# Performance work log

Hardware: AMD Instinct MI355X
Metric: run time of the kernel (lower is better)

## Reference

```python
import jax, jax.numpy as jnp
import numpy as np

N_NODES = 100000
N_BATCH = 16384
N_EDGES = 524288
D_FEAT = 256


def setup_inputs() -> dict:
    key = jax.random.key(0)
    k1, k2, k3, k4 = jax.random.split(key, 4)
    features = jax.random.normal(k1, (N_NODES, D_FEAT), dtype=jnp.float32)
    # flat ragged neighbor list: neigh_idx[e] is a node id, segment_ids[e] is
    # the batch-node it belongs to (sorted, i.e. CSR-style ragged layout)
    neigh_idx = jax.random.randint(k2, (N_EDGES,), 0, N_NODES, dtype=jnp.int64)
    segment_ids = jnp.sort(jax.random.randint(k3, (N_EDGES,), 0, N_BATCH, dtype=jnp.int64))
    self_feats = jax.random.normal(k4, (N_BATCH, D_FEAT), dtype=jnp.float32)
    return {"features": features, "neigh_idx": neigh_idx,
            "segment_ids": segment_ids, "self_feats": self_feats}


def reference(features, neigh_idx, segment_ids, self_feats):
    B = self_feats.shape[0]
    # gather neighbor embeddings [E, D] and segment-mean them per batch node.
    # This is the sparse equivalent of the original's dense mask.mm(embed_matrix)
    # where mask rows were already divided by the neighbor count.
    gathered = features[neigh_idx]                                   # [E, D]
    sums = jax.ops.segment_sum(gathered, segment_ids, num_segments=B)  # [B, D]
    counts = jax.ops.segment_sum(jnp.ones((neigh_idx.shape[0],), features.dtype),
                                 segment_ids, num_segments=B)          # [B]
    agg_feats = sums / jnp.maximum(counts, 1.0)[:, None]             # [B, D]
    diff_feats = self_feats - agg_feats
    return jnp.concatenate((diff_feats, agg_feats), axis=1)          # [B, 2D]
```

## Files before the change

### kernel.cpp

```cpp
#include <hip/hip_runtime.h>

#define D_FEAT 256

__device__ __forceinline__ unsigned short f2bf_rn(float f) {
    unsigned int u = __float_as_uint(f);
    u += 0x7FFFu + ((u >> 16) & 1u);
    return (unsigned short)(u >> 16);
}

__global__ __launch_bounds__(256) void prep_kernel(
    const float* __restrict__ features,
    const int*   __restrict__ seg,
    unsigned short* __restrict__ fbf,
    int*         __restrict__ offs,
    long long n4,
    int E, int B, int convBlocks)
{
    if ((int)blockIdx.x < convBlocks) {
        long long i = (long long)blockIdx.x * 256 + threadIdx.x;
        const long long stride = (long long)convBlocks * 256;
        const float4* src = (const float4*)features;
        ushort4* dst = (ushort4*)fbf;
        for (; i < n4; i += stride) {
            float4 v = src[i];
            ushort4 o;
            o.x = f2bf_rn(v.x); o.y = f2bf_rn(v.y);
            o.z = f2bf_rn(v.z); o.w = f2bf_rn(v.w);
            dst[i] = o;
        }
    } else {
        int b = ((int)blockIdx.x - convBlocks) * 256 + threadIdx.x;
        if (b <= B) {
            int lo = 0, hi = E;
            while (lo < hi) {
                int mid = (lo + hi) >> 1;
                if (seg[mid] < b) lo = mid + 1; else hi = mid;
            }
            offs[b] = lo;
        }
    }
}

__global__ __launch_bounds__(256) void intra_agg_bf16(
    const unsigned short* __restrict__ fbf,
    const int*   __restrict__ neigh,
    const int*   __restrict__ offs,
    const float* __restrict__ self_feats,
    float*       __restrict__ out,
    int B)
{
    const int s    = blockIdx.x * 4 + (threadIdx.x >> 6);
    const int lane = threadIdx.x & 63;
    if (s >= B) return;

    const int start = __builtin_amdgcn_readfirstlane(offs[s]);
    const int end   = __builtin_amdgcn_readfirstlane(offs[s + 1]);
    const int count = end - start;

    float a0 = 0.f, a1 = 0.f, a2 = 0.f, a3 = 0.f;
    float c0 = 0.f, c1 = 0.f, c2 = 0.f, c3 = 0.f;

    int e = start;
    for (; e + 8 <= end; e += 8) {
        int n[8];
        #pragma unroll
        for (int i = 0; i < 8; ++i) n[i] = neigh[e + i];
        uint2 v[8];
        #pragma unroll
        for (int i = 0; i < 8; ++i)
            v[i] = *(const uint2*)(fbf + (size_t)n[i] * D_FEAT + (lane << 2));
        #pragma unroll
        for (int i = 0; i < 8; i += 2) {
            a0 += __uint_as_float(v[i].x << 16);
            a1 += __uint_as_float(v[i].x & 0xFFFF0000u);
            a2 += __uint_as_float(v[i].y << 16);
            a3 += __uint_as_float(v[i].y & 0xFFFF0000u);
            c0 += __uint_as_float(v[i + 1].x << 16);
            c1 += __uint_as_float(v[i + 1].x & 0xFFFF0000u);
            c2 += __uint_as_float(v[i + 1].y << 16);
            c3 += __uint_as_float(v[i + 1].y & 0xFFFF0000u);
        }
    }
    for (; e < end; ++e) {
        int n = neigh[e];
        uint2 v = *(const uint2*)(fbf + (size_t)n * D_FEAT + (lane << 2));
        a0 += __uint_as_float(v.x << 16);
        a1 += __uint_as_float(v.x & 0xFFFF0000u);
        a2 += __uint_as_float(v.y << 16);
        a3 += __uint_as_float(v.y & 0xFFFF0000u);
    }
    a0 += c0; a1 += c1; a2 += c2; a3 += c3;

    const float inv = 1.0f / fmaxf((float)count, 1.0f);
    float4 agg;
    agg.x = a0 * inv; agg.y = a1 * inv; agg.z = a2 * inv; agg.w = a3 * inv;

    const float4 self = ((const float4*)(self_feats + (size_t)s * D_FEAT))[lane];
    float4 diff;
    diff.x = self.x - agg.x; diff.y = self.y - agg.y;
    diff.z = self.z - agg.z; diff.w = self.w - agg.w;

    float4* o = (float4*)(out + (size_t)s * 2 * D_FEAT);
    o[lane]      = diff;
    o[64 + lane] = agg;
}

__global__ __launch_bounds__(256) void seg_offsets_kernel(
    const int* __restrict__ seg, int* __restrict__ offs, int E, int B)
{
    int b = blockIdx.x * blockDim.x + threadIdx.x;
    if (b > B) return;
    int lo = 0, hi = E;
    while (lo < hi) {
        int mid = (lo + hi) >> 1;
        if (seg[mid] < b) lo = mid + 1; else hi = mid;
    }
    offs[b] = lo;
}

__global__ __launch_bounds__(256) void intra_agg_main(
    const float* __restrict__ features,
    const int*   __restrict__ neigh,
    const int*   __restrict__ offs,
    const float* __restrict__ self_feats,
    float*       __restrict__ out,
    int B)
{
    const int s    = blockIdx.x * 4 + (threadIdx.x >> 6);
    const int lane = threadIdx.x & 63;
    if (s >= B) return;

    const int start = offs[s];
    const int end   = offs[s + 1];
    const int count = end - start;

    float4 a0 = make_float4(0.f,0.f,0.f,0.f);
    float4 a1 = make_float4(0.f,0.f,0.f,0.f);
    int e = start;
    for (; e + 2 <= end; e += 2) {
        int n0 = neigh[e], n1 = neigh[e + 1];
        float4 v0 = ((const float4*)(features + (size_t)n0 * D_FEAT))[lane];
        float4 v1 = ((const float4*)(features + (size_t)n1 * D_FEAT))[lane];
        a0.x += v0.x; a0.y += v0.y; a0.z += v0.z; a0.w += v0.w;
        a1.x += v1.x; a1.y += v1.y; a1.z += v1.z; a1.w += v1.w;
    }
    for (; e < end; ++e) {
        int n = neigh[e];
        float4 v = ((const float4*)(features + (size_t)n * D_FEAT))[lane];
        a0.x += v.x; a0.y += v.y; a0.z += v.z; a0.w += v.w;
    }
    a0.x += a1.x; a0.y += a1.y; a0.z += a1.z; a0.w += a1.w;

    const float inv = 1.0f / fmaxf((float)count, 1.0f);
    float4 agg;
    agg.x = a0.x * inv; agg.y = a0.y * inv; agg.z = a0.z * inv; agg.w = a0.w * inv;
    const float4 self = ((const float4*)(self_feats + (size_t)s * D_FEAT))[lane];
    float4 diff;
    diff.x = self.x - agg.x; diff.y = self.y - agg.y;
    diff.z = self.z - agg.z; diff.w = self.w - agg.w;
    float4* o = (float4*)(out + (size_t)s * 2 * D_FEAT);
    o[lane]      = diff;
    o[64 + lane] = agg;
}

extern "C" void kernel_launch(void* const* d_in, const int* in_sizes, int n_in,
                              void* d_out, int out_size, void* d_ws, size_t ws_size,
                              hipStream_t stream) {
    const float* features    = (const float*)d_in[0];
    const int*   neigh_idx   = (const int*)d_in[1];
    const int*   segment_ids = (const int*)d_in[2];
    const float* self_feats  = (const float*)d_in[3];
    float*       out         = (float*)d_out;

    const int E = in_sizes[1];
    const int B = in_sizes[3] / D_FEAT;
    const long long NF = (long long)in_sizes[0];

    const size_t offs_bytes = (((size_t)(B + 2) * 4) + 255) & ~(size_t)255;
    const size_t need = offs_bytes + (size_t)NF * 2;

    int* offs = (int*)d_ws;

    if (ws_size >= need) {
        unsigned short* fbf = (unsigned short*)((char*)d_ws + offs_bytes);
        const int convBlocks = 4096;
        const int offsBlocks = (B + 1 + 255) / 256;
        prep_kernel<<<convBlocks + offsBlocks, 256, 0, stream>>>(
            features, segment_ids, fbf, offs, NF / 4, E, B, convBlocks);
        intra_agg_bf16<<<(B + 3) / 4, 256, 0, stream>>>(
            fbf, neigh_idx, offs, self_feats, out, B);
    } else {
        seg_offsets_kernel<<<(B + 1 + 255) / 256, 256, 0, stream>>>(
            segment_ids, offs, E, B);
        intra_agg_main<<<(B + 3) / 4, 256, 0, stream>>>(
            features, neigh_idx, offs, self_feats, out, B);
    }
}
```

Baseline: 221.5 us.

## Split wavefront into half-waves gathering two rows with 16-byte loads

The bf16 aggregation kernel now has each half of a 64-lane wavefront handle a different neighbor row. Each lane loads 16 bytes (8 bf16 values) instead of 8, and the two halves are combined with a cross-lane shuffle at the end. Only the first half then writes the output, using nontemporal stores, and the fp32-to-bf16 conversion pass uses nontemporal loads. The aim is wider memory transactions and fewer gather instructions, at the cost of a shuffle reduction and half the lanes idling during the epilogue.

```diff
diff --git a/kernel.cpp b/kernel.cpp
--- a/kernel.cpp
+++ b/kernel.cpp
@@ -1,6 +1,9 @@
 #include <hip/hip_runtime.h>
 
 #define D_FEAT 256
+
+typedef float  f32x4 __attribute__((ext_vector_type(4)));
+typedef unsigned int u32x4 __attribute__((ext_vector_type(4)));
 
 __device__ __forceinline__ unsigned short f2bf_rn(float f) {
     unsigned int u = __float_as_uint(f);
@@ -19,10 +22,10 @@
     if ((int)blockIdx.x < convBlocks) {
         long long i = (long long)blockIdx.x * 256 + threadIdx.x;
         const long long stride = (long long)convBlocks * 256;
-        const float4* src = (const float4*)features;
+        const f32x4* src = (const f32x4*)features;
         ushort4* dst = (ushort4*)fbf;
         for (; i < n4; i += stride) {
-            float4 v = src[i];
+            f32x4 v = __builtin_nontemporal_load(src + i);
             ushort4 o;
             o.x = f2bf_rn(v.x); o.y = f2bf_rn(v.y);
             o.z = f2bf_rn(v.z); o.w = f2bf_rn(v.w);
@@ -51,58 +54,88 @@
 {
     const int s    = blockIdx.x * 4 + (threadIdx.x >> 6);
     const int lane = threadIdx.x & 63;
+    const int half = lane >> 5;
+    const int hl   = lane & 31;
     if (s >= B) return;
 
     const int start = __builtin_amdgcn_readfirstlane(offs[s]);
     const int end   = __builtin_amdgcn_readfirstlane(offs[s + 1]);
     const int count = end - start;
 
-    float a0 = 0.f, a1 = 0.f, a2 = 0.f, a3 = 0.f;
-    float c0 = 0.f, c1 = 0.f, c2 = 0.f, c3 = 0.f;
+    float acc[8];
+    #pragma unroll
+    for (int k = 0; k < 8; ++k) acc[k] = 0.f;
+
+    const int elem = hl << 3;
 
     int e = start;
     for (; e + 8 <= end; e += 8) {
-        int n[8];
+        int n0 = neigh[e + 0 + half];
+        int n1 = neigh[e + 2 + half];
+        int n2 = neigh[e + 4 + half];
+        int n3 = neigh[e + 6 + half];
+        u32x4 v0 = *(const u32x4*)(fbf + (size_t)n0 * D_FEAT + elem);
+        u32x4 v1 = *(const u32x4*)(fbf + (size_t)n1 * D_FEAT + elem);
+        u32x4 v2 = *(const u32x4*)(fbf + (size_t)n2 * D_FEAT + elem);
+        u32x4 v3 = *(const u32x4*)(fbf + (size_t)n3 * D_FEAT + elem);
+        u32x4 vs[4] = {v0, v1, v2, v3};
         #pragma unroll
-        for (int i = 0; i < 8; ++i) n[i] = neigh[e + i];
-        uint2 v[8];
-        #pragma unroll
-        for (int i = 0; i < 8; ++i)
-            v[i] = *(const uint2*)(fbf + (size_t)n[i] * D_FEAT + (lane << 2));
-        #pragma unroll
-        for (int i = 0; i < 8; i += 2) {
-            a0 += __uint_as_float(v[i].x << 16);
-            a1 += __uint_as_float(v[i].x & 0xFFFF0000u);
-            a2 += __uint_as_float(v[i].y << 16);
-            a3 += __uint_as_float(v[i].y & 0xFFFF0000u);
-            c0 += __uint_as_float(v[i + 1].x << 16);
-            c1 += __uint_as_float(v[i + 1].x & 0xFFFF0000u);
-            c2 += __uint_as_float(v[i + 1].y << 16);
-            c3 += __uint_as_float(v[i + 1].y & 0xFFFF0000u);
+        for (int i = 0; i < 4; ++i) {
+            acc[0] += __uint_as_float(vs[i].x << 16);
+            acc[1] += __uint_as_float(vs[i].x & 0xFFFF0000u);
+            acc[2] += __uint_as_float(vs[i].y << 16);
+            acc[3] += __uint_as_float(vs[i].y & 0xFFFF0000u);
+            acc[4] += __uint_as_float(vs[i].z << 16);
+            acc[5] += __uint_as_float(vs[i].z & 0xFFFF0000u);
+            acc[6] += __uint_as_float(vs[i].w << 16);
+            acc[7] += __uint_as_float(vs[i].w & 0xFFFF0000u);
         }
     }
-    for (; e < end; ++e) {
+    for (; e + 2 <= end; e += 2) {
+        int n = neigh[e + half];
+        u32x4 v = *(const u32x4*)(fbf + (size_t)n * D_FEAT + elem);
+        acc[0] += __uint_as_float(v.x << 16);
+        acc[1] += __uint_as_float(v.x & 0xFFFF0000u);
+        acc[2] += __uint_as_float(v.y << 16);
+        acc[3] += __uint_as_float(v.y & 0xFFFF0000u);
+        acc[4] += __uint_as_float(v.z << 16);
+        acc[5] += __uint_as_float(v.z & 0xFFFF0000u);
+        acc[6] += __uint_as_float(v.w << 16);
+        acc[7] += __uint_as_float(v.w & 0xFFFF0000u);
+    }
+    if (e < end && half == 0) {
         int n = neigh[e];
-        uint2 v = *(const uint2*)(fbf + (size_t)n * D_FEAT + (lane << 2));
-        a0 += __uint_as_float(v.x << 16);
-        a1 += __uint_as_float(v.x & 0xFFFF0000u);
-        a2 += __uint_as_float(v.y << 16);
-        a3 += __uint_as_float(v.y & 0xFFFF0000u);
-    }
-    a0 += c0; a1 += c1; a2 += c2; a3 += c3;
-
-    const float inv = 1.0f / fmaxf((float)count, 1.0f);
-    float4 agg;
-    agg.x = a0 * inv; agg.y = a1 * inv; agg.z = a2 * inv; agg.w = a3 * inv;
-
-    const float4 self = ((const float4*)(self_feats + (size_t)s * D_FEAT))[lane];
-    float4 diff;
-    diff.x = self.x - agg.x; diff.y = self.y - agg.y;
-    diff.z = self.z - agg.z; diff.w = self.w - agg.w;
-
-    float4* o = (float4*)(out + (size_t)s * 2 * D_FEAT);
-    o[lane]      = diff;
-    o[64 + lane] = agg;
+        u32x4 v = *(const u32x4*)(fbf + (size_t)n * D_FEAT + elem);
+        acc[0] += __uint_as_float(v.x << 16);
+        acc[1] += __uint_as_float(v.x & 0xFFFF0000u);
+        acc[2] += __uint_as_float(v.y << 16);
+        acc[3] += __uint_as_float(v.y & 0xFFFF0000u);
+        acc[4] += __uint_as_float(v.z << 16);
+        acc[5] += __uint_as_float(v.z & 0xFFFF0000u);
+        acc[6] += __uint_as_float(v.w << 16);
+        acc[7] += __uint_as_float(v.w & 0xFFFF0000u);
+    }
+
+    #pragma unroll
+    for (int k = 0; k < 8; ++k)
+        acc[k] += __shfl_xor(acc[k], 32, 64);
+
+    if (half == 0) {
+        const float inv = 1.0f / fmaxf((float)count, 1.0f);
+        const f32x4* selfp = (const f32x4*)(self_feats + (size_t)s * D_FEAT + elem);
+        f32x4 s0 = selfp[0];
+        f32x4 s1 = selfp[1];
+        f32x4 g0 = { acc[0] * inv, acc[1] * inv, acc[2] * inv, acc[3] * inv };
+        f32x4 g1 = { acc[4] * inv, acc[5] * inv, acc[6] * inv, acc[7] * inv };
+        f32x4 d0 = { s0.x - g0.x, s0.y - g0.y, s0.z - g0.z, s0.w - g0.w };
+        f32x4 d1 = { s1.x - g1.x, s1.y - g1.y, s1.z - g1.z, s1.w - g1.w };
+
+        float* ob = out + (size_t)s * 2 * D_FEAT;
+        __builtin_nontemporal_store(d0, (f32x4*)(ob + elem));
+        __builtin_nontemporal_store(d1, (f32x4*)(ob + elem + 4));
+        __builtin_nontemporal_store(g0, (f32x4*)(ob + D_FEAT + elem));
+        __builtin_nontemporal_store(g1, (f32x4*)(ob + D_FEAT + elem + 4));
+    }
 }
 
 __global__ __launch_bounds__(256) void seg_offsets_kernel(
```

Measured after the change: 216.8 us. -2.1%, faster.
